# Performance work log

Hardware: AMD Instinct MI355X
Metric: run time of the kernel (lower is better)

The kernel has to match this reference:

```python
import jax, jax.numpy as jnp
import numpy as np

NEG_BIG = -1e10
EPS = 1e-12  # F.normalize default eps


def l2_normalize(x, axis=-1):
    # matches torch.nn.functional.normalize(x): x / max(||x||_2, eps)
    n = jnp.sqrt(jnp.sum(x * x, axis=axis, keepdims=True))
    return x / jnp.maximum(n, EPS)


def setup_inputs() -> dict:
    key = jax.random.key(0)
    k1, k2, k3 = jax.random.split(key, 3)
    B, S, T, D, R = 16, 512, 512, 512, 8
    return {
        "src_emb": jax.random.normal(k1, (B, S, D), dtype=jnp.float32),
        "tar_emb": jax.random.normal(k2, (B, T, D), dtype=jnp.float32),
        "src_mask": jnp.ones((B, S), dtype=jnp.float32),
        "tar_mask": jnp.ones((B, T), dtype=jnp.float32),
        "mul_score_w": jax.random.normal(k3, (R, D), dtype=jnp.float32),
    }


def reference(src_emb, tar_emb, src_mask, tar_mask, mul_score_w):
    # w: [R, D] row-normalized relation vectors
    w = l2_normalize(mul_score_w, axis=-1)
    # rank-1 diagonal projections per relation
    src_wt = jnp.einsum("bsd,rd->brs", src_emb, w)          # [B,R,S]
    tar_wt = jnp.einsum("btd,rd->brt", tar_emb, w)          # [B,R,T]
    src_map = src_wt[..., None] * w[None, :, None, :]        # [B,R,S,D]
    tar_map = tar_wt[..., None] * w[None, :, None, :]        # [B,R,T,D]
    # attention scores per relation
    score = jnp.einsum("brsd,brtd->brst", src_map, tar_map)  # [B,R,S,T]
    pair_mask = src_mask[:, :, None] * tar_mask[:, None, :]  # [B,S,T]
    score = score + ((1.0 - pair_mask) * NEG_BIG)[:, None, :, :]
    weight = jax.nn.softmax(score, axis=3)                   # softmax over tar
    # sum over rel and tar in one contraction (avoids 5D tensor)
    out = jnp.einsum("brst,brtd->bsd", weight, tar_map)      # [B,S,D]
    return out
```

## Files before the change

### kernel.cpp

```cpp
#include <hip/hip_runtime.h>
#include <hip/hip_bf16.h>
#include <math.h>

#define B 16
#define Sn 512
#define Tn 512
#define Dn 512
#define Rn 8
#define NEG_BIG (-1e10f)

__global__ __launch_bounds__(512) void norm_w_kernel(
    const float* __restrict__ w_in, float* __restrict__ w_out,
    float* __restrict__ g_out) {
  int lane = threadIdx.x & 63;
  int r = threadIdx.x >> 6;
  float x[8];
  float ss = 0.f;
#pragma unroll
  for (int j = 0; j < 8; ++j) {
    x[j] = w_in[r * Dn + 64 * j + lane];
    ss += x[j] * x[j];
  }
#pragma unroll
  for (int off = 32; off; off >>= 1) ss += __shfl_xor(ss, off, 64);
  float n = sqrtf(ss);
  float inv = 1.0f / fmaxf(n, 1e-12f);
#pragma unroll
  for (int j = 0; j < 8; ++j) w_out[r * Dn + 64 * j + lane] = x[j] * inv;
  if (lane == 0) g_out[r] = ss * inv * inv;
}

__global__ __launch_bounds__(256) void proj_kernel(
    const float* __restrict__ emb, const float* __restrict__ w,
    float* __restrict__ wt) {
  __shared__ float4 w4[Rn * 128];
  const float4* wg = (const float4*)w;
  for (int i = threadIdx.x; i < Rn * 128; i += 256) w4[i] = wg[i];
  __syncthreads();

  int wid = threadIdx.x >> 6, lane = threadIdx.x & 63;
  int row = blockIdx.x * 4 + wid;
  const float4* e4 = (const float4*)(emb + (size_t)row * Dn);
  float4 xa = e4[lane];
  float4 xb = e4[lane + 64];

  float p[8];
#pragma unroll
  for (int r = 0; r < 8; ++r) {
    float4 wa = w4[r * 128 + lane];
    float4 wb = w4[r * 128 + lane + 64];
    p[r] = xa.x * wa.x + xa.y * wa.y + xa.z * wa.z + xa.w * wa.w +
           xb.x * wb.x + xb.y * wb.y + xb.z * wb.z + xb.w * wb.w;
  }
#pragma unroll
  for (int off = 32; off; off >>= 1) {
#pragma unroll
    for (int r = 0; r < 8; ++r) p[r] += __shfl_xor(p[r], off, 64);
  }
  if (lane == 0) {
    int b = row >> 9, n = row & 511;
#pragma unroll
    for (int r = 0; r < 8; ++r) wt[(((size_t)b * Rn + r) << 9) + n] = p[r];
  }
}

__global__ __launch_bounds__(256) void softmax_kernel(
    const float* __restrict__ src_wt, const float* __restrict__ tar_wt,
    const float* __restrict__ src_mask, const float* __restrict__ tar_mask,
    const float* __restrict__ g, float* __restrict__ cbuf) {
  int pair = blockIdx.x >> 4;
  int chunk = blockIdx.x & 15;
  int b = pair >> 3, r = pair & 7;

  __shared__ float tw_s[Tn], tm_s[Tn];
  for (int i = threadIdx.x; i < Tn; i += 256) {
    tw_s[i] = tar_wt[((size_t)pair << 9) + i];
    tm_s[i] = tar_mask[((size_t)b << 9) + i];
  }
  __syncthreads();

  int wid = threadIdx.x >> 6, lane = threadIdx.x & 63;
  float gr = g[r];
  float tw[8], tmn[8];
#pragma unroll
  for (int j = 0; j < 8; ++j) {
    tw[j] = tw_s[lane + 64 * j];
    tmn[j] = tm_s[lane + 64 * j];
  }

  for (int i = 0; i < 8; ++i) {
    int s = chunk * 32 + wid * 8 + i;
    float sw = src_wt[((size_t)pair << 9) + s];
    float sm = src_mask[((size_t)b << 9) + s];
    float a = gr * sw;
    float sc[8];
    float m = -INFINITY;
#pragma unroll
    for (int j = 0; j < 8; ++j) {
      sc[j] = a * tw[j] + (1.0f - sm * tmn[j]) * NEG_BIG;
      m = fmaxf(m, sc[j]);
    }
#pragma unroll
    for (int off = 32; off; off >>= 1) m = fmaxf(m, __shfl_xor(m, off, 64));
    float ps = 0.f, wsum = 0.f;
#pragma unroll
    for (int j = 0; j < 8; ++j) {
      float p = __expf(sc[j] - m);
      ps += p;
      wsum += p * tw[j];
    }
#pragma unroll
    for (int off = 32; off; off >>= 1) {
      ps += __shfl_xor(ps, off, 64);
      wsum += __shfl_xor(wsum, off, 64);
    }
    if (lane == 0) cbuf[((size_t)pair << 9) + s] = wsum / ps;
  }
}

__global__ __launch_bounds__(256) void out_kernel(
    const float* __restrict__ cbuf, const float* __restrict__ w,
    float* __restrict__ out) {
  __shared__ float4 w4[Rn * 128];
  const float4* wg = (const float4*)w;
  for (int i = threadIdx.x; i < Rn * 128; i += 256) w4[i] = wg[i];
  __syncthreads();

  int wid = threadIdx.x >> 6, lane = threadIdx.x & 63;
  int row = blockIdx.x * 4 + wid;
  int b = row >> 9, s = row & 511;

  float cv[8];
#pragma unroll
  for (int r = 0; r < 8; ++r)
    cv[r] = cbuf[(((size_t)b * Rn + r) << 9) + s];

  float4 a0 = {0, 0, 0, 0}, a1 = {0, 0, 0, 0};
#pragma unroll
  for (int r = 0; r < 8; ++r) {
    float4 wa = w4[r * 128 + lane];
    float4 wb = w4[r * 128 + lane + 64];
    a0.x += cv[r] * wa.x; a0.y += cv[r] * wa.y;
    a0.z += cv[r] * wa.z; a0.w += cv[r] * wa.w;
    a1.x += cv[r] * wb.x; a1.y += cv[r] * wb.y;
    a1.z += cv[r] * wb.z; a1.w += cv[r] * wb.w;
  }
  float4* o4 = (float4*)(out + (size_t)row * Dn);
  o4[lane] = a0;
  o4[lane + 64] = a1;
}

extern "C" void kernel_launch(void* const* d_in, const int* in_sizes, int n_in,
                              void* d_out, int out_size, void* d_ws,
                              size_t ws_size, hipStream_t stream) {
  const float* src_emb = (const float*)d_in[0];
  const float* tar_emb = (const float*)d_in[1];
  const float* src_mask = (const float*)d_in[2];
  const float* tar_mask = (const float*)d_in[3];
  const float* w_in = (const float*)d_in[4];
  float* out = (float*)d_out;

  float* ws = (float*)d_ws;
  float* w_norm = ws;
  float* g = ws + 4096;
  float* src_wt = ws + 4112;
  float* tar_wt = ws + 69648;
  float* cbuf = ws + 135184;

  norm_w_kernel<<<1, 512, 0, stream>>>(w_in, w_norm, g);
  proj_kernel<<<(B * Sn) / 4, 256, 0, stream>>>(src_emb, w_norm, src_wt);
  proj_kernel<<<(B * Tn) / 4, 256, 0, stream>>>(tar_emb, w_norm, tar_wt);
  softmax_kernel<<<B * Rn * (Sn / 32), 256, 0, stream>>>(
      src_wt, tar_wt, src_mask, tar_mask, g, cbuf);
  out_kernel<<<(B * Sn) / 4, 256, 0, stream>>>(cbuf, w_norm, out);
}
```

Before: 119.8 us.

## Fuse weight normalization, projections, softmax and output into two kernels

```diff
diff --git a/kernel.cpp b/kernel.cpp
--- a/kernel.cpp
+++ b/kernel.cpp
@@ -9,37 +9,65 @@
 #define Rn 8
 #define NEG_BIG (-1e10f)
 
-__global__ __launch_bounds__(512) void norm_w_kernel(
-    const float* __restrict__ w_in, float* __restrict__ w_out,
-    float* __restrict__ g_out) {
-  int lane = threadIdx.x & 63;
-  int r = threadIdx.x >> 6;
-  float x[8];
-  float ss = 0.f;
-#pragma unroll
-  for (int j = 0; j < 8; ++j) {
-    x[j] = w_in[r * Dn + 64 * j + lane];
-    ss += x[j] * x[j];
-  }
-#pragma unroll
-  for (int off = 32; off; off >>= 1) ss += __shfl_xor(ss, off, 64);
-  float n = sqrtf(ss);
-  float inv = 1.0f / fmaxf(n, 1e-12f);
-#pragma unroll
-  for (int j = 0; j < 8; ++j) w_out[r * Dn + 64 * j + lane] = x[j] * inv;
-  if (lane == 0) g_out[r] = ss * inv * inv;
+__device__ __forceinline__ float wred_sum(float v) {
+#pragma unroll
+  for (int off = 32; off; off >>= 1) v += __shfl_xor(v, off, 64);
+  return v;
+}
+__device__ __forceinline__ float wred_max(float v) {
+#pragma unroll
+  for (int off = 32; off; off >>= 1) v = fmaxf(v, __shfl_xor(v, off, 64));
+  return v;
+}
+
+__device__ __forceinline__ void stage_norm_w(const float* __restrict__ w,
+                                             float4* w4n, float* gs) {
+  const float4* wg = (const float4*)w;
+  int wid = threadIdx.x >> 6, lane = threadIdx.x & 63;
+  int base = wid * 256;
+  float4 g0 = wg[base + lane];
+  float4 g1 = wg[base + 64 + lane];
+  float4 g2 = wg[base + 128 + lane];
+  float4 g3 = wg[base + 192 + lane];
+  float ss0 = g0.x * g0.x + g0.y * g0.y + g0.z * g0.z + g0.w * g0.w +
+              g1.x * g1.x + g1.y * g1.y + g1.z * g1.z + g1.w * g1.w;
+  float ss1 = g2.x * g2.x + g2.y * g2.y + g2.z * g2.z + g2.w * g2.w +
+              g3.x * g3.x + g3.y * g3.y + g3.z * g3.z + g3.w * g3.w;
+  ss0 = wred_sum(ss0);
+  ss1 = wred_sum(ss1);
+  float inv0 = 1.0f / fmaxf(sqrtf(ss0), 1e-12f);
+  float inv1 = 1.0f / fmaxf(sqrtf(ss1), 1e-12f);
+  float4 o;
+  o.x = g0.x * inv0; o.y = g0.y * inv0; o.z = g0.z * inv0; o.w = g0.w * inv0;
+  w4n[base + lane] = o;
+  o.x = g1.x * inv0; o.y = g1.y * inv0; o.z = g1.z * inv0; o.w = g1.w * inv0;
+  w4n[base + 64 + lane] = o;
+  o.x = g2.x * inv1; o.y = g2.y * inv1; o.z = g2.z * inv1; o.w = g2.w * inv1;
+  w4n[base + 128 + lane] = o;
+  o.x = g3.x * inv1; o.y = g3.y * inv1; o.z = g3.z * inv1; o.w = g3.w * inv1;
+  w4n[base + 192 + lane] = o;
+  if (lane == 0) {
+    gs[2 * wid] = ss0 * inv0 * inv0;
+    gs[2 * wid + 1] = ss1 * inv1 * inv1;
+  }
 }
 
 __global__ __launch_bounds__(256) void proj_kernel(
-    const float* __restrict__ emb, const float* __restrict__ w,
-    float* __restrict__ wt) {
-  __shared__ float4 w4[Rn * 128];
-  const float4* wg = (const float4*)w;
-  for (int i = threadIdx.x; i < Rn * 128; i += 256) w4[i] = wg[i];
+    const float* __restrict__ src_emb, const float* __restrict__ tar_emb,
+    const float* __restrict__ w, float* __restrict__ src_wt,
+    float* __restrict__ tar_wt) {
+  __shared__ float4 w4n[Rn * 128];
+  __shared__ float gs[Rn];
+  stage_norm_w(w, w4n, gs);
   __syncthreads();
 
+  bool is_src = blockIdx.x < 2048;
+  const float* emb = is_src ? src_emb : tar_emb;
+  float* wt = is_src ? src_wt : tar_wt;
+  int bb = is_src ? blockIdx.x : blockIdx.x - 2048;
+
   int wid = threadIdx.x >> 6, lane = threadIdx.x & 63;
-  int row = blockIdx.x * 4 + wid;
+  int row = bb * 4 + wid;
   const float4* e4 = (const float4*)(emb + (size_t)row * Dn);
   float4 xa = e4[lane];
   float4 xb = e4[lane + 64];
@@ -47,8 +75,8 @@
   float p[8];
 #pragma unroll
   for (int r = 0; r < 8; ++r) {
-    float4 wa = w4[r * 128 + lane];
-    float4 wb = w4[r * 128 + lane + 64];
+    float4 wa = w4n[r * 128 + lane];
+    float4 wb = w4n[r * 128 + 64 + lane];
     p[r] = xa.x * wa.x + xa.y * wa.y + xa.z * wa.z + xa.w * wa.w +
            xb.x * wb.x + xb.y * wb.y + xb.z * wb.z + xb.w * wb.w;
   }
@@ -64,90 +92,96 @@
   }
 }
 
-__global__ __launch_bounds__(256) void softmax_kernel(
+__global__ __launch_bounds__(256) void fused_kernel(
     const float* __restrict__ src_wt, const float* __restrict__ tar_wt,
     const float* __restrict__ src_mask, const float* __restrict__ tar_mask,
-    const float* __restrict__ g, float* __restrict__ cbuf) {
-  int pair = blockIdx.x >> 4;
-  int chunk = blockIdx.x & 15;
-  int b = pair >> 3, r = pair & 7;
-
-  __shared__ float tw_s[Tn], tm_s[Tn];
-  for (int i = threadIdx.x; i < Tn; i += 256) {
-    tw_s[i] = tar_wt[((size_t)pair << 9) + i];
-    tm_s[i] = tar_mask[((size_t)b << 9) + i];
+    const float* __restrict__ w, float* __restrict__ out) {
+  __shared__ float4 w4n[Rn * 128];
+  __shared__ float gs[Rn];
+  __shared__ float sw_s[Rn][8];
+  __shared__ float sm_s[8];
+
+  int b = blockIdx.x >> 6;
+  int s0 = (blockIdx.x & 63) * 8;
+
+  stage_norm_w(w, w4n, gs);
+  if (threadIdx.x < 64) {
+    int r = threadIdx.x >> 3, si = threadIdx.x & 7;
+    sw_s[r][si] = src_wt[(((size_t)b * Rn + r) << 9) + s0 + si];
+    if (r == 0) sm_s[si] = src_mask[((size_t)b << 9) + s0 + si];
   }
   __syncthreads();
 
   int wid = threadIdx.x >> 6, lane = threadIdx.x & 63;
-  float gr = g[r];
-  float tw[8], tmn[8];
-#pragma unroll
-  for (int j = 0; j < 8; ++j) {
-    tw[j] = tw_s[lane + 64 * j];
-    tmn[j] = tm_s[lane + 64 * j];
-  }
-
-  for (int i = 0; i < 8; ++i) {
-    int s = chunk * 32 + wid * 8 + i;
-    float sw = src_wt[((size_t)pair << 9) + s];
-    float sm = src_mask[((size_t)b << 9) + s];
-    float a = gr * sw;
-    float sc[8];
-    float m = -INFINITY;
-#pragma unroll
-    for (int j = 0; j < 8; ++j) {
-      sc[j] = a * tw[j] + (1.0f - sm * tmn[j]) * NEG_BIG;
-      m = fmaxf(m, sc[j]);
+
+  const float4* twb = (const float4*)(tar_wt + ((size_t)b << 12));
+  float4 tw[8][2];
+#pragma unroll
+  for (int r = 0; r < 8; ++r) {
+    tw[r][0] = twb[r * 128 + lane];
+    tw[r][1] = twb[r * 128 + 64 + lane];
+  }
+  const float4* tmb = (const float4*)(tar_mask + ((size_t)b << 9));
+  float4 tm0 = tmb[lane], tm1 = tmb[lane + 64];
+  float gr[8];
+#pragma unroll
+  for (int r = 0; r < 8; ++r) gr[r] = gs[r];
+
+#pragma unroll
+  for (int it = 0; it < 2; ++it) {
+    int sl = wid * 2 + it;
+    int s = s0 + sl;
+    float sm = sm_s[sl];
+    float mk[8];
+    mk[0] = (1.0f - sm * tm0.x) * NEG_BIG;
+    mk[1] = (1.0f - sm * tm0.y) * NEG_BIG;
+    mk[2] = (1.0f - sm * tm0.z) * NEG_BIG;
+    mk[3] = (1.0f - sm * tm0.w) * NEG_BIG;
+    mk[4] = (1.0f - sm * tm1.x) * NEG_BIG;
+    mk[5] = (1.0f - sm * tm1.y) * NEG_BIG;
+    mk[6] = (1.0f - sm * tm1.z) * NEG_BIG;
+    mk[7] = (1.0f - sm * tm1.w) * NEG_BIG;
+
+    float cacc[8];
+#pragma unroll
+    for (int r = 0; r < 8; ++r) {
+      float a = gr[r] * sw_s[r][sl];
+      float twv[8] = {tw[r][0].x, tw[r][0].y, tw[r][0].z, tw[r][0].w,
+                      tw[r][1].x, tw[r][1].y, tw[r][1].z, tw[r][1].w};
+      float sc[8];
+      float m = -INFINITY;
+#pragma unroll
+      for (int k = 0; k < 8; ++k) {
+        sc[k] = a * twv[k] + mk[k];
+        m = fmaxf(m, sc[k]);
+      }
+      m = wred_max(m);
+      float ps = 0.f, wsum = 0.f;
+#pragma unroll
+      for (int k = 0; k < 8; ++k) {
+        float p = __expf(sc[k] - m);
+        ps += p;
+        wsum += p * twv[k];
+      }
+      ps = wred_sum(ps);
+      wsum = wred_sum(wsum);
+      cacc[r] = wsum / ps;
     }
-#pragma unroll
-    for (int off = 32; off; off >>= 1) m = fmaxf(m, __shfl_xor(m, off, 64));
-    float ps = 0.f, wsum = 0.f;
-#pragma unroll
-    for (int j = 0; j < 8; ++j) {
-      float p = __expf(sc[j] - m);
-      ps += p;
-      wsum += p * tw[j];
+
+    float4 o0 = {0, 0, 0, 0}, o1 = {0, 0, 0, 0};
+#pragma unroll
+    for (int r = 0; r < 8; ++r) {
+      float4 wa = w4n[r * 128 + lane];
+      float4 wb = w4n[r * 128 + 64 + lane];
+      o0.x += cacc[r] * wa.x; o0.y += cacc[r] * wa.y;
+      o0.z += cacc[r] * wa.z; o0.w += cacc[r] * wa.w;
+      o1.x += cacc[r] * wb.x; o1.y += cacc[r] * wb.y;
+      o1.z += cacc[r] * wb.z; o1.w += cacc[r] * wb.w;
     }
-#pragma unroll
-    for (int off = 32; off; off >>= 1) {
-      ps += __shfl_xor(ps, off, 64);
-      wsum += __shfl_xor(wsum, off, 64);
-    }
-    if (lane == 0) cbuf[((size_t)pair << 9) + s] = wsum / ps;
-  }
-}
-
-__global__ __launch_bounds__(256) void out_kernel(
-    const float* __restrict__ cbuf, const float* __restrict__ w,
-    float* __restrict__ out) {
-  __shared__ float4 w4[Rn * 128];
-  const float4* wg = (const float4*)w;
-  for (int i = threadIdx.x; i < Rn * 128; i += 256) w4[i] = wg[i];
-  __syncthreads();
-
-  int wid = threadIdx.x >> 6, lane = threadIdx.x & 63;
-  int row = blockIdx.x * 4 + wid;
-  int b = row >> 9, s = row & 511;
-
-  float cv[8];
-#pragma unroll
-  for (int r = 0; r < 8; ++r)
-    cv[r] = cbuf[(((size_t)b * Rn + r) << 9) + s];
-
-  float4 a0 = {0, 0, 0, 0}, a1 = {0, 0, 0, 0};
-#pragma unroll
-  for (int r = 0; r < 8; ++r) {
-    float4 wa = w4[r * 128 + lane];
-    float4 wb = w4[r * 128 + lane + 64];
-    a0.x += cv[r] * wa.x; a0.y += cv[r] * wa.y;
-    a0.z += cv[r] * wa.z; a0.w += cv[r] * wa.w;
-    a1.x += cv[r] * wb.x; a1.y += cv[r] * wb.y;
-    a1.z += cv[r] * wb.z; a1.w += cv[r] * wb.w;
-  }
-  float4* o4 = (float4*)(out + (size_t)row * Dn);
-  o4[lane] = a0;
-  o4[lane + 64] = a1;
+    float4* dst = (float4*)(out + (((size_t)b << 9) + s) * Dn);
+    dst[lane] = o0;
+    dst[lane + 64] = o1;
+  }
 }
 
 extern "C" void kernel_launch(void* const* d_in, const int* in_sizes, int n_in,
@@ -161,16 +195,10 @@
   float* out = (float*)d_out;
 
   float* ws = (float*)d_ws;
-  float* w_norm = ws;
-  float* g = ws + 4096;
-  float* src_wt = ws + 4112;
-  float* tar_wt = ws + 69648;
-  float* cbuf = ws + 135184;
-
-  norm_w_kernel<<<1, 512, 0, stream>>>(w_in, w_norm, g);
-  proj_kernel<<<(B * Sn) / 4, 256, 0, stream>>>(src_emb, w_norm, src_wt);
-  proj_kernel<<<(B * Tn) / 4, 256, 0, stream>>>(tar_emb, w_norm, tar_wt);
-  softmax_kernel<<<B * Rn * (Sn / 32), 256, 0, stream>>>(
-      src_wt, tar_wt, src_mask, tar_mask, g, cbuf);
-  out_kernel<<<(B * Sn) / 4, 256, 0, stream>>>(cbuf, w_norm, out);
-}
+  float* src_wt = ws;
+  float* tar_wt = ws + 65536;
+
+  proj_kernel<<<4096, 256, 0, stream>>>(src_emb, tar_emb, w_in, src_wt, tar_wt);
+  fused_kernel<<<B * 64, 256, 0, stream>>>(src_wt, tar_wt, src_mask, tar_mask,
+                                           w_in, out);
+}
```

After: 116.8 us. -2.5%, faster.
